# Kernel tuning notes

Hardware: AMD Instinct MI355X
Metric: run time of the kernel (lower is better)

## Reference

```python
import jax, jax.numpy as jnp
import numpy as np

N_NODES = 100000
N_EDGES = 1600000
F_IN = 128
HID = 128
N_CLASSES = 32
N_GRAPHS = 1024


def setup_inputs() -> dict:
    key = jax.random.key(0)
    ks = jax.random.split(key, 8)
    x = jax.random.normal(ks[0], (N_NODES, F_IN), dtype=jnp.float32)
    edge_index = jax.random.randint(ks[1], (2, N_EDGES), 0, N_NODES, dtype=jnp.int64)
    batch = jnp.sort(jax.random.randint(ks[2], (N_NODES,), 0, N_GRAPHS, dtype=jnp.int64))
    W1 = jax.random.normal(ks[3], (F_IN, HID), dtype=jnp.float32) * (1.0 / np.sqrt(F_IN))
    b1 = jnp.zeros((HID,), dtype=jnp.float32)
    W2 = jax.random.normal(ks[4], (HID, HID), dtype=jnp.float32) * (1.0 / np.sqrt(HID))
    b2 = jnp.zeros((HID,), dtype=jnp.float32)
    Wf = jax.random.normal(ks[5], (HID, N_CLASSES), dtype=jnp.float32) * (1.0 / np.sqrt(HID))
    bf = jnp.zeros((N_CLASSES,), dtype=jnp.float32)
    return {"x": x, "edge_index": edge_index, "batch": batch,
            "W1": W1, "b1": b1, "W2": W2, "b2": b2, "Wf": Wf, "bf": bf}


def _gcn_conv(x, W, b, src, dst, n_nodes):
    # GCNConv: linear transform, add self-loops, symmetric normalization,
    # scatter-add aggregation, then bias.
    h = x @ W                                   # [N, H]
    loop = jnp.arange(n_nodes, dtype=src.dtype)
    s = jnp.concatenate([src, loop])            # [E+N]
    d = jnp.concatenate([dst, loop])
    deg = jax.ops.segment_sum(jnp.ones_like(d, dtype=h.dtype), d, num_segments=n_nodes)
    dinv = jnp.where(deg > 0, jax.lax.rsqrt(deg), jnp.zeros_like(deg))
    norm = dinv[s] * dinv[d]                    # [E+N]
    msgs = h[s] * norm[:, None]                 # gather + scale
    out = jax.ops.segment_sum(msgs, d, num_segments=n_nodes)  # scatter-add
    return out + b


def reference(x, edge_index, batch, W1, b1, W2, b2, Wf, bf):
    src, dst = edge_index[0], edge_index[1]
    n = x.shape[0]
    h = _gcn_conv(x, W1, b1, src, dst, n)
    h = jax.nn.relu(h)
    # F.dropout(training=False) -> identity (inference baseline)
    h = _gcn_conv(h, W2, b2, src, dst, n)
    # global_mean_pool over graph ids
    pooled_sum = jax.ops.segment_sum(h, batch, num_segments=N_GRAPHS)       # [G, H]
    counts = jax.ops.segment_sum(jnp.ones((n,), h.dtype), batch, num_segments=N_GRAPHS)
    pooled = pooled_sum / jnp.clip(counts, 1.0)[:, None]
    return pooled @ Wf + bf                      # [G, C]
```

## Files before the change

### kernel.cpp

```cpp
#include <hip/hip_runtime.h>
#include <hip/hip_bf16.h>

#define N_NODES   100000
#define N_EDGES   1600000
#define FDIM      128
#define N_GRAPHS  1024
#define N_CLASSES 32
#define SCAN_BLK  1024
#define M_PAD     100032

typedef __attribute__((ext_vector_type(8))) short short8v;
typedef __attribute__((ext_vector_type(4))) float f32x4;

__device__ __forceinline__ float bflo(unsigned u){ union{unsigned i; float f;} c; c.i = u << 16; return c.f; }
__device__ __forceinline__ float bfhi(unsigned u){ union{unsigned i; float f;} c; c.i = u & 0xffff0000u; return c.f; }
__device__ __forceinline__ unsigned short f2bf(float f){
    union{float f; unsigned u;} c{f};
    return (unsigned short)((c.u + 0x7fffu + ((c.u >> 16) & 1u)) >> 16);
}
__device__ __forceinline__ unsigned packbf2(float a, float b){
    return (unsigned)f2bf(a) | ((unsigned)f2bf(b) << 16);
}

__device__ __forceinline__ void fma8(float* acc, float w, uint4 u) {
    acc[0] += w * bflo(u.x); acc[1] += w * bfhi(u.x);
    acc[2] += w * bflo(u.y); acc[3] += w * bfhi(u.y);
    acc[4] += w * bflo(u.z); acc[5] += w * bfhi(u.z);
    acc[6] += w * bflo(u.w); acc[7] += w * bfhi(u.w);
}

__global__ void k_f2bf(const float* __restrict__ in, unsigned* __restrict__ out, int n2) {
    int i = blockIdx.x * blockDim.x + threadIdx.x;
    if (i < n2) {
        float2 v = ((const float2*)in)[i];
        out[i] = packbf2(v.x, v.y);
    }
}

__global__ void k_wt(const float* __restrict__ W, unsigned short* __restrict__ Wt) {
    int i = blockIdx.x * blockDim.x + threadIdx.x;
    int k = i >> 7, n = i & 127;
    Wt[n * 128 + k] = f2bf(W[i]);
}

__global__ void k_count(const int* __restrict__ dst, int* __restrict__ indeg, int E) {
    int i = blockIdx.x * blockDim.x + threadIdx.x;
    if (i < E) atomicAdd(&indeg[dst[i]], 1);
}

__global__ void k_dinv(const int* __restrict__ indeg, float* __restrict__ dinv, int n) {
    int i = blockIdx.x * blockDim.x + threadIdx.x;
    if (i < n) dinv[i] = rsqrtf((float)(indeg[i] + 1));
}

__global__ void k_scan1(const int* __restrict__ in, int* __restrict__ out,
                        int* __restrict__ bsums, int n) {
    __shared__ int lds[256];
    int blk = blockIdx.x, t = threadIdx.x;
    int base = blk * SCAN_BLK + t * 4;
    int v[4];
#pragma unroll
    for (int i = 0; i < 4; ++i) v[i] = (base + i < n) ? in[base + i] : 0;
    int local = v[0] + v[1] + v[2] + v[3];
    lds[t] = local;
    __syncthreads();
    for (int off = 1; off < 256; off <<= 1) {
        int x = lds[t];
        int y = (t >= off) ? lds[t - off] : 0;
        __syncthreads();
        lds[t] = x + y;
        __syncthreads();
    }
    int excl = lds[t] - local;
    if (t == 255) bsums[blk] = lds[255];
    int run = excl;
#pragma unroll
    for (int i = 0; i < 4; ++i) {
        if (base + i < n) { out[base + i] = run; run += v[i]; }
    }
}

__global__ void k_scan2(int* __restrict__ bsums, int nb) {
    __shared__ int lds[256];
    int t = threadIdx.x;
    int orig = (t < nb) ? bsums[t] : 0;
    lds[t] = orig;
    __syncthreads();
    for (int off = 1; off < 256; off <<= 1) {
        int x = lds[t];
        int y = (t >= off) ? lds[t - off] : 0;
        __syncthreads();
        lds[t] = x + y;
        __syncthreads();
    }
    if (t < nb) bsums[t] = lds[t] - orig;
}

__global__ void k_scan3(int* __restrict__ rp, const int* __restrict__ boffs, int n, int E) {
    int i = blockIdx.x * blockDim.x + threadIdx.x;
    if (i < n) rp[i] += boffs[i / SCAN_BLK];
    if (i == n) rp[n] = E;
}

__global__ void k_fill(const int* __restrict__ src, const int* __restrict__ dst,
                       const int* __restrict__ rp, int* __restrict__ cursor,
                       int* __restrict__ col, float* __restrict__ wgt,
                       const float* __restrict__ dinv, int E) {
    int i = blockIdx.x * blockDim.x + threadIdx.x;
    if (i < E) {
        int d = dst[i], s = src[i];
        int p = atomicAdd(&cursor[d], 1);
        int idx = rp[d] + p;
        col[idx] = s;
        wgt[idx] = dinv[d] * dinv[s];
    }
}

#define AGG3_BODY(X2)                                                            \
    int lane = threadIdx.x & 63;                                                 \
    int grp  = lane >> 4;                                                        \
    int fl   = lane & 15;                                                        \
    int v = (blockIdx.x << 2) + (threadIdx.x >> 6);                              \
    if (v >= N_NODES) return;                                                    \
    float dv = dinv[v];                                                          \
    int e0 = rp[v];                                                              \
    int L  = rp[v + 1] - e0 + 1;                               \
    float acc[8] = {0.f,0.f,0.f,0.f,0.f,0.f,0.f,0.f};                            \
    int i = grp;                                                                 \
    int sA = -1, sB = -1; float wA = 0.f, wB = 0.f;                              \
    if (i < L) {                                                                 \
        if (i == 0) { sA = v; wA = dv * dv; }                                    \
        else        { sA = col[e0 + i - 1]; wA = wgt[e0 + i - 1]; }              \
    }                                                                            \
    if (i + 4 < L) { sB = col[e0 + i + 3]; wB = wgt[e0 + i + 3]; }               \
    while (sA >= 0) {                                                            \
        int sC = -1, sD = -1; float wC = 0.f, wD = 0.f;                          \
        if (i + 8  < L) { sC = col[e0 + i + 7];  wC = wgt[e0 + i + 7]; }         \
        if (i + 12 < L) { sD = col[e0 + i + 11]; wD = wgt[e0 + i + 11]; }        \
        uint4 uA = *(const uint4*)(X2 + (size_t)sA * 64 + fl * 4);               \
        uint4 uB;                                                                \
        bool hB = (sB >= 0);                                                     \
        if (hB) uB = *(const uint4*)(X2 + (size_t)sB * 64 + fl * 4);             \
        fma8(acc, wA, uA);                                                       \
        if (hB) fma8(acc, wB, uB);                                               \
        i += 8; sA = sC; wA = wC; sB = sD; wB = wD;                              \
    }                                                                            \
    _Pragma("unroll")                                                            \
    for (int j = 0; j < 8; ++j) {                                                \
        acc[j] += __shfl_xor(acc[j], 16, 64);                                    \
        acc[j] += __shfl_xor(acc[j], 32, 64);                                    \
    }

__global__ __launch_bounds__(256) void k_agg1(
    const unsigned* __restrict__ X2, unsigned* __restrict__ O2,
    const int* __restrict__ rp, const int* __restrict__ col,
    const float* __restrict__ wgt, const float* __restrict__ dinv)
{
    AGG3_BODY(X2)
    if (grp == 0) {
        uint4 o;
        o.x = packbf2(acc[0], acc[1]);
        o.y = packbf2(acc[2], acc[3]);
        o.z = packbf2(acc[4], acc[5]);
        o.w = packbf2(acc[6], acc[7]);
        *(uint4*)(O2 + (size_t)v * 64 + fl * 4) = o;
    }
}

__global__ __launch_bounds__(256) void k_agg2(
    const unsigned* __restrict__ X2,
    const int* __restrict__ rp, const int* __restrict__ col,
    const float* __restrict__ wgt, const float* __restrict__ dinv,
    const int* __restrict__ batch, float* __restrict__ P, int* __restrict__ cnt)
{
    AGG3_BODY(X2)
    int g = batch[v];
    atomicAdd(&P[(size_t)g * FDIM + fl * 8 + 2 * grp],     acc[2 * grp]);
    atomicAdd(&P[(size_t)g * FDIM + fl * 8 + 2 * grp + 1], acc[2 * grp + 1]);
    if (lane == 0) atomicAdd(&cnt[g], 1);
}

__global__ __launch_bounds__(256) void k_gemm_mfma(
    const unsigned short* __restrict__ A, const unsigned short* __restrict__ Wt,
    const float* __restrict__ bias, unsigned short* __restrict__ B)
{
    int lane = threadIdx.x & 63;
    int wv = threadIdx.x >> 6;
    size_t row0 = (size_t)blockIdx.x * 64 + (size_t)wv * 16;
    int r = lane & 15, g = lane >> 4;

    short8v af[4];
    const unsigned short* arow = A + (row0 + r) * FDIM + g * 8;
#pragma unroll
    for (int ks = 0; ks < 4; ++ks)
        af[ks] = *(const short8v*)(arow + ks * 32);

    f32x4 acc[8];
#pragma unroll
    for (int ct = 0; ct < 8; ++ct) {
        f32x4 a = {0.f, 0.f, 0.f, 0.f};
        const unsigned short* wrow = Wt + (ct * 16 + r) * FDIM + g * 8;
#pragma unroll
        for (int ks = 0; ks < 4; ++ks) {
            short8v bfr = *(const short8v*)(wrow + ks * 32);
            a = __builtin_amdgcn_mfma_f32_16x16x32_bf16(af[ks], bfr, a, 0, 0, 0);
        }
        acc[ct] = a;
    }

#pragma unroll
    for (int ct = 0; ct < 8; ++ct) {
        int c = ct * 16 + r;
        float bs = bias[c];
#pragma unroll
        for (int i = 0; i < 4; ++i) {
            size_t row = row0 + g * 4 + i;
            if (row < N_NODES) {
                float vv = fmaxf(acc[ct][i] + bs, 0.f);
                B[row * FDIM + c] = f2bf(vv);
            }
        }
    }
}

__global__ void k_wcomb(const float* __restrict__ W2, const float* __restrict__ Wf,
                        const float* __restrict__ b2, const float* __restrict__ bf,
                        float* __restrict__ Wc, float* __restrict__ bc) {
    int idx = blockIdx.x * blockDim.x + threadIdx.x;
    if (idx < 128 * 32) {
        int k = idx >> 5, c = idx & 31;
        float acc = 0.0f;
        for (int m = 0; m < 128; ++m) acc += W2[k * 128 + m] * Wf[m * 32 + c];
        Wc[idx] = acc;
    }
    if (idx < 32) {
        float acc = bf[idx];
        for (int m = 0; m < 128; ++m) acc += b2[m] * Wf[m * 32 + idx];
        bc[idx] = acc;
    }
}

__global__ void k_final(const float* __restrict__ P, const int* __restrict__ cnt,
                        const float* __restrict__ Wc, const float* __restrict__ bc,
                        const float* __restrict__ bf, float* __restrict__ out) {
    __shared__ float p[128];
    int g = blockIdx.x, t = threadIdx.x;
    int c_ = cnt[g];
    float inv = (c_ > 0) ? 1.0f / (float)c_ : 0.0f;
    p[t] = P[(size_t)g * FDIM + t] * inv;
    __syncthreads();
    if (t < N_CLASSES) {
        float acc = (c_ > 0) ? bc[t] : bf[t];
#pragma unroll
        for (int k = 0; k < 128; ++k) acc = fmaf(p[k], Wc[k * 32 + t], acc);
        out[(size_t)g * N_CLASSES + t] = acc;
    }
}

extern "C" void kernel_launch(void* const* d_in, const int* in_sizes, int n_in,
                              void* d_out, int out_size, void* d_ws, size_t ws_size,
                              hipStream_t stream) {
    const float* x    = (const float*)d_in[0];
    const int*   ei   = (const int*)d_in[1];
    const int*   batch= (const int*)d_in[2];
    const float* W1   = (const float*)d_in[3];
    const float* b1   = (const float*)d_in[4];
    const float* W2   = (const float*)d_in[5];
    const float* b2   = (const float*)d_in[6];
    const float* Wf   = (const float*)d_in[7];
    const float* bf   = (const float*)d_in[8];
    const int* src = ei;
    const int* dst = ei + N_EDGES;

    char* w = (char*)d_ws;
    auto alloc = [&](size_t bytes) { char* p = w; w += (bytes + 255) & ~255ull; return p; };
    int*      indeg  = (int*)     alloc((size_t)N_NODES * 4);
    float*    dinv   = (float*)   alloc((size_t)N_NODES * 4);
    int*      rp     = (int*)     alloc((size_t)(N_NODES + 1) * 4);
    int*      cursor = (int*)     alloc((size_t)N_NODES * 4);
    int*      bsums  = (int*)     alloc(1024 * 4);
    int*      col    = (int*)     alloc((size_t)N_EDGES * 4);
    float*    wgt    = (float*)   alloc((size_t)N_EDGES * 4);
    unsigned* xh     = (unsigned*)alloc((size_t)N_NODES * 64 * 4);
    unsigned* Ab     = (unsigned*)alloc((size_t)M_PAD  * 64 * 4);
    unsigned* Bb     = (unsigned*)alloc((size_t)N_NODES * 64 * 4);
    unsigned short* Wt = (unsigned short*)alloc(128 * 128 * 2);
    float*    P      = (float*)   alloc((size_t)N_GRAPHS * FDIM * 4);
    int*      cnt    = (int*)     alloc((size_t)N_GRAPHS * 4);
    float*    Wc     = (float*)   alloc(128 * 32 * 4);
    float*    bc     = (float*)   alloc(32 * 4);

    hipMemsetAsync(indeg,  0, (size_t)N_NODES * 4, stream);
    hipMemsetAsync(cursor, 0, (size_t)N_NODES * 4, stream);
    hipMemsetAsync(P,      0, (size_t)N_GRAPHS * FDIM * 4, stream);
    hipMemsetAsync(cnt,    0, (size_t)N_GRAPHS * 4, stream);

    const int nbScan = (N_NODES + SCAN_BLK - 1) / SCAN_BLK;

    k_f2bf<<<(N_NODES * 64 + 255) / 256, 256, 0, stream>>>(x, xh, N_NODES * 64);
    k_wt  <<<64, 256, 0, stream>>>(W1, Wt);

    k_count<<<(N_EDGES + 255) / 256, 256, 0, stream>>>(dst, indeg, N_EDGES);
    k_dinv <<<(N_NODES + 255) / 256, 256, 0, stream>>>(indeg, dinv, N_NODES);
    k_scan1<<<nbScan, 256, 0, stream>>>(indeg, rp, bsums, N_NODES);
    k_scan2<<<1, 256, 0, stream>>>(bsums, nbScan);
    k_scan3<<<(N_NODES + 1 + 255) / 256, 256, 0, stream>>>(rp, bsums, N_NODES, N_EDGES);
    k_fill <<<(N_EDGES + 255) / 256, 256, 0, stream>>>(src, dst, rp, cursor, col, wgt, dinv, N_EDGES);

    k_agg1<<<(N_NODES + 3) / 4, 256, 0, stream>>>(xh, Ab, rp, col, wgt, dinv);
    k_gemm_mfma<<<M_PAD / 64, 256, 0, stream>>>((const unsigned short*)Ab, Wt, b1,
                                                (unsigned short*)Bb);

    k_wcomb<<<16, 256, 0, stream>>>(W2, Wf, b2, bf, Wc, bc);

    k_agg2<<<(N_NODES + 3) / 4, 256, 0, stream>>>(Bb, rp, col, wgt, dinv, batch, P, cnt);

    k_final<<<N_GRAPHS, 128, 0, stream>>>(P, cnt, Wc, bc, bf, (float*)d_out);
}
```

Measured before the change: 492.5 us.

## Slice feature matrices into 8 column slabs and interleave CSR edge records

Node feature arrays are stored as eight 16-feature slices, each contiguous across nodes. The aggregation kernels become one block per (4-node group, slice), so each pass over a slice gathers from a 3.2 MB working set that may stay in cache. Column indices and edge weights are packed into one 8-byte record read with nontemporal loads, and the GEMM reads and writes the sliced layout. The trade-off is that edge lists are traversed eight times, each gather is only 32 bytes per row, and there are many more blocks.

```diff
diff --git a/kernel.cpp b/kernel.cpp
--- a/kernel.cpp
+++ b/kernel.cpp
@@ -8,6 +8,7 @@
 #define N_CLASSES 32
 #define SCAN_BLK  1024
 #define M_PAD     100032
+#define SLICE_U   (M_PAD * 8)
 
 typedef __attribute__((ext_vector_type(8))) short short8v;
 typedef __attribute__((ext_vector_type(4))) float f32x4;
@@ -21,19 +22,17 @@
 __device__ __forceinline__ unsigned packbf2(float a, float b){
     return (unsigned)f2bf(a) | ((unsigned)f2bf(b) << 16);
 }
-
-__device__ __forceinline__ void fma8(float* acc, float w, uint4 u) {
-    acc[0] += w * bflo(u.x); acc[1] += w * bfhi(u.x);
-    acc[2] += w * bflo(u.y); acc[3] += w * bfhi(u.y);
-    acc[4] += w * bflo(u.z); acc[5] += w * bfhi(u.z);
-    acc[6] += w * bflo(u.w); acc[7] += w * bfhi(u.w);
+__device__ __forceinline__ long long ldnt64(const void* p){
+    return __builtin_nontemporal_load((const long long*)p);
 }
 
 __global__ void k_f2bf(const float* __restrict__ in, unsigned* __restrict__ out, int n2) {
     int i = blockIdx.x * blockDim.x + threadIdx.x;
     if (i < n2) {
-        float2 v = ((const float2*)in)[i];
-        out[i] = packbf2(v.x, v.y);
+        float2 v2 = ((const float2*)in)[i];
+        int v = i >> 6, jp = i & 63;
+        int f = jp >> 3, off = jp & 7;
+        out[(size_t)f * SLICE_U + (size_t)v * 8 + off] = packbf2(v2.x, v2.y);
     }
 }
 
@@ -104,80 +103,75 @@
 
 __global__ void k_fill(const int* __restrict__ src, const int* __restrict__ dst,
                        const int* __restrict__ rp, int* __restrict__ cursor,
-                       int* __restrict__ col, float* __restrict__ wgt,
-                       const float* __restrict__ dinv, int E) {
+                       int2* __restrict__ edges, const float* __restrict__ dinv, int E) {
     int i = blockIdx.x * blockDim.x + threadIdx.x;
     if (i < E) {
         int d = dst[i], s = src[i];
         int p = atomicAdd(&cursor[d], 1);
-        int idx = rp[d] + p;
-        col[idx] = s;
-        wgt[idx] = dinv[d] * dinv[s];
-    }
-}
-
-#define AGG3_BODY(X2)                                                            \
+        int2 r; r.x = s; r.y = __float_as_int(dinv[d] * dinv[s]);
+        edges[rp[d] + p] = r;
+    }
+}
+
+#define AGGS_BODY(X2)                                                            \
     int lane = threadIdx.x & 63;                                                 \
-    int grp  = lane >> 4;                                                        \
-    int fl   = lane & 15;                                                        \
-    int v = (blockIdx.x << 2) + (threadIdx.x >> 6);                              \
-    if (v >= N_NODES) return;                                                    \
+    int wv   = threadIdx.x >> 6;                                                 \
+    int f    = blockIdx.x & 7;                                                   \
+    int v    = ((blockIdx.x >> 3) << 2) + wv;                                    \
+    int grp  = lane >> 3;                                                        \
+    int fl   = lane & 7;                                                         \
+    const unsigned* Xs = X2 + (size_t)f * SLICE_U;                               \
     float dv = dinv[v];                                                          \
-    int e0 = rp[v];                                                              \
-    int L  = rp[v + 1] - e0 + 1;                               \
-    float acc[8] = {0.f,0.f,0.f,0.f,0.f,0.f,0.f,0.f};                            \
+    int e0 = rp[v], deg = rp[v + 1] - e0;                                        \
+    float a0 = 0.f, a1 = 0.f;                                                    \
+    if (grp == 0) {                                                              \
+        unsigned u = Xs[(size_t)v * 8 + fl];                                     \
+        float ws = dv * dv;                                                      \
+        a0 = ws * bflo(u); a1 = ws * bfhi(u);                                    \
+    }                                                                            \
     int i = grp;                                                                 \
-    int sA = -1, sB = -1; float wA = 0.f, wB = 0.f;                              \
-    if (i < L) {                                                                 \
-        if (i == 0) { sA = v; wA = dv * dv; }                                    \
-        else        { sA = col[e0 + i - 1]; wA = wgt[e0 + i - 1]; }              \
-    }                                                                            \
-    if (i + 4 < L) { sB = col[e0 + i + 3]; wB = wgt[e0 + i + 3]; }               \
-    while (sA >= 0) {                                                            \
-        int sC = -1, sD = -1; float wC = 0.f, wD = 0.f;                          \
-        if (i + 8  < L) { sC = col[e0 + i + 7];  wC = wgt[e0 + i + 7]; }         \
-        if (i + 12 < L) { sD = col[e0 + i + 11]; wD = wgt[e0 + i + 11]; }        \
-        uint4 uA = *(const uint4*)(X2 + (size_t)sA * 64 + fl * 4);               \
-        uint4 uB;                                                                \
-        bool hB = (sB >= 0);                                                     \
-        if (hB) uB = *(const uint4*)(X2 + (size_t)sB * 64 + fl * 4);             \
-        fma8(acc, wA, uA);                                                       \
-        if (hB) fma8(acc, wB, uB);                                               \
-        i += 8; sA = sC; wA = wC; sB = sD; wB = wD;                              \
+    bool h0 = (i < deg);                                                         \
+    long long rec = 0;                                                           \
+    if (h0) rec = ldnt64(edges + e0 + i);                                        \
+    while (h0) {                                                                 \
+        bool h1 = (i + 8 < deg);                                                 \
+        long long rec1 = 0;                                                      \
+        if (h1) rec1 = ldnt64(edges + e0 + i + 8);                               \
+        int s   = (int)(rec & 0xffffffffll);                                     \
+        float w = __int_as_float((int)(rec >> 32));                              \
+        unsigned u = Xs[(size_t)s * 8 + fl];                                     \
+        a0 += w * bflo(u); a1 += w * bfhi(u);                                    \
+        i += 8; rec = rec1; h0 = h1;                                             \
     }                                                                            \
     _Pragma("unroll")                                                            \
-    for (int j = 0; j < 8; ++j) {                                                \
-        acc[j] += __shfl_xor(acc[j], 16, 64);                                    \
-        acc[j] += __shfl_xor(acc[j], 32, 64);                                    \
-    }
-
-__global__ __launch_bounds__(256) void k_agg1(
+    for (int off = 8; off < 64; off <<= 1) {                                     \
+        a0 += __shfl_xor(a0, off, 64);                                           \
+        a1 += __shfl_xor(a1, off, 64);                                           \
+    }
+
+__global__ __launch_bounds__(256) void k_aggs1(
     const unsigned* __restrict__ X2, unsigned* __restrict__ O2,
-    const int* __restrict__ rp, const int* __restrict__ col,
-    const float* __restrict__ wgt, const float* __restrict__ dinv)
+    const int* __restrict__ rp, const int2* __restrict__ edges,
+    const float* __restrict__ dinv)
 {
-    AGG3_BODY(X2)
+    AGGS_BODY(X2)
+    if (grp == 0)
+        O2[(size_t)f * SLICE_U + (size_t)v * 8 + fl] = packbf2(a0, a1);
+}
+
+__global__ __launch_bounds__(256) void k_aggs2(
+    const unsigned* __restrict__ X2,
+    const int* __restrict__ rp, const int2* __restrict__ edges,
+    const float* __restrict__ dinv, const int* __restrict__ batch,
+    float* __restrict__ P, int* __restrict__ cnt)
+{
+    AGGS_BODY(X2)
+    int g = batch[v];
     if (grp == 0) {
-        uint4 o;
-        o.x = packbf2(acc[0], acc[1]);
-        o.y = packbf2(acc[2], acc[3]);
-        o.z = packbf2(acc[4], acc[5]);
-        o.w = packbf2(acc[6], acc[7]);
-        *(uint4*)(O2 + (size_t)v * 64 + fl * 4) = o;
-    }
-}
-
-__global__ __launch_bounds__(256) void k_agg2(
-    const unsigned* __restrict__ X2,
-    const int* __restrict__ rp, const int* __restrict__ col,
-    const float* __restrict__ wgt, const float* __restrict__ dinv,
-    const int* __restrict__ batch, float* __restrict__ P, int* __restrict__ cnt)
-{
-    AGG3_BODY(X2)
-    int g = batch[v];
-    atomicAdd(&P[(size_t)g * FDIM + fl * 8 + 2 * grp],     acc[2 * grp]);
-    atomicAdd(&P[(size_t)g * FDIM + fl * 8 + 2 * grp + 1], acc[2 * grp + 1]);
-    if (lane == 0) atomicAdd(&cnt[g], 1);
+        atomicAdd(&P[(size_t)g * FDIM + f * 16 + fl * 2],     a0);
+        atomicAdd(&P[(size_t)g * FDIM + f * 16 + fl * 2 + 1], a1);
+    }
+    if (f == 0 && lane == 0) atomicAdd(&cnt[g], 1);
 }
 
 __global__ __launch_bounds__(256) void k_gemm_mfma(
@@ -190,10 +184,12 @@
     int r = lane & 15, g = lane >> 4;
 
     short8v af[4];
-    const unsigned short* arow = A + (row0 + r) * FDIM + g * 8;
-#pragma unroll
-    for (int ks = 0; ks < 4; ++ks)
-        af[ks] = *(const short8v*)(arow + ks * 32);
+#pragma unroll
+    for (int ks = 0; ks < 4; ++ks) {
+        int fa  = 2 * ks + (g >> 1);
+        int off = (g & 1) * 8;
+        af[ks] = *(const short8v*)(A + (size_t)fa * SLICE_U * 2 + (row0 + r) * 16 + off);
+    }
 
     f32x4 acc[8];
 #pragma unroll
@@ -210,14 +206,13 @@
 
 #pragma unroll
     for (int ct = 0; ct < 8; ++ct) {
-        int c = ct * 16 + r;
-        float bs = bias[c];
+        float bs = bias[ct * 16 + r];
 #pragma unroll
         for (int i = 0; i < 4; ++i) {
             size_t row = row0 + g * 4 + i;
             if (row < N_NODES) {
                 float vv = fmaxf(acc[ct][i] + bs, 0.f);
-                B[row * FDIM + c] = f2bf(vv);
+                B[(size_t)ct * SLICE_U * 2 + row * 16 + r] = f2bf(vv);
             }
         }
     }
@@ -279,11 +274,10 @@
     int*      rp     = (int*)     alloc((size_t)(N_NODES + 1) * 4);
     int*      cursor = (int*)     alloc((size_t)N_NODES * 4);
     int*      bsums  = (int*)     alloc(1024 * 4);
-    int*      col    = (int*)     alloc((size_t)N_EDGES * 4);
-    float*    wgt    = (float*)   alloc((size_t)N_EDGES * 4);
-    unsigned* xh     = (unsigned*)alloc((size_t)N_NODES * 64 * 4);
-    unsigned* Ab     = (unsigned*)alloc((size_t)M_PAD  * 64 * 4);
-    unsigned* Bb     = (unsigned*)alloc((size_t)N_NODES * 64 * 4);
+    int2*     edges  = (int2*)    alloc((size_t)N_EDGES * 8);
+    unsigned* xh     = (unsigned*)alloc((size_t)SLICE_U * 8 * 4);
+    unsigned* Ab     = (unsigned*)alloc((size_t)SLICE_U * 8 * 4);
+    unsigned* Bb     = (unsigned*)alloc((size_t)SLICE_U * 8 * 4);
     unsigned short* Wt = (unsigned short*)alloc(128 * 128 * 2);
     float*    P      = (float*)   alloc((size_t)N_GRAPHS * FDIM * 4);
     int*      cnt    = (int*)     alloc((size_t)N_GRAPHS * 4);
@@ -305,15 +299,15 @@
     k_scan1<<<nbScan, 256, 0, stream>>>(indeg, rp, bsums, N_NODES);
     k_scan2<<<1, 256, 0, stream>>>(bsums, nbScan);
     k_scan3<<<(N_NODES + 1 + 255) / 256, 256, 0, stream>>>(rp, bsums, N_NODES, N_EDGES);
-    k_fill <<<(N_EDGES + 255) / 256, 256, 0, stream>>>(src, dst, rp, cursor, col, wgt, dinv, N_EDGES);
-
-    k_agg1<<<(N_NODES + 3) / 4, 256, 0, stream>>>(xh, Ab, rp, col, wgt, dinv);
+    k_fill <<<(N_EDGES + 255) / 256, 256, 0, stream>>>(src, dst, rp, cursor, edges, dinv, N_EDGES);
+
+    k_aggs1<<<(N_NODES / 4) * 8, 256, 0, stream>>>(xh, Ab, rp, edges, dinv);
     k_gemm_mfma<<<M_PAD / 64, 256, 0, stream>>>((const unsigned short*)Ab, Wt, b1,
                                                 (unsigned short*)Bb);
 
     k_wcomb<<<16, 256, 0, stream>>>(W2, Wf, b2, bf, Wc, bc);
 
-    k_agg2<<<(N_NODES + 3) / 4, 256, 0, stream>>>(Bb, rp, col, wgt, dinv, batch, P, cnt);
+    k_aggs2<<<(N_NODES / 4) * 8, 256, 0, stream>>>(Bb, rp, edges, dinv, batch, P, cnt);
 
     k_final<<<N_GRAPHS, 128, 0, stream>>>(P, cnt, Wc, bc, bf, (float*)d_out);
 }
```

New measurement: 1.536 ms. +211.8%, slower.

## Replace second-layer aggregation with source-ordered scatter-to-graph pooling

Applied to the files above, without the earlier changes.

The second GCN layer is only needed through its mean pool, so the pooled sum is computed directly as a weighted sum of source-node features into graph bins. A source-sorted edge list (including self-loops) holds packed weight and destination-graph id, and chunked blocks accumulate into LDS before a partial-sum reduction. This removes the per-node gather-aggregate pass and its global atomics. In exchange it adds an out-degree count, a second scan and fill pass, larger workspace, and packs the graph id into the low mantissa bits of the weight, which slightly perturbs precision.

```diff
diff --git a/kernel.cpp b/kernel.cpp
--- a/kernel.cpp
+++ b/kernel.cpp
@@ -8,6 +8,8 @@
 #define N_CLASSES 32
 #define SCAN_BLK  1024
 #define M_PAD     100032
+#define CHUNK     1563
+#define NCHUNK    64
 
 typedef __attribute__((ext_vector_type(8))) short short8v;
 typedef __attribute__((ext_vector_type(4))) float f32x4;
@@ -21,6 +23,9 @@
 __device__ __forceinline__ unsigned packbf2(float a, float b){
     return (unsigned)f2bf(a) | ((unsigned)f2bf(b) << 16);
 }
+__device__ __forceinline__ int packgw(float w, int g){
+    return (__float_as_int(w) & ~1023) | g;
+}
 
 __device__ __forceinline__ void fma8(float* acc, float w, uint4 u) {
     acc[0] += w * bflo(u.x); acc[1] += w * bfhi(u.x);
@@ -43,14 +48,19 @@
     Wt[n * 128 + k] = f2bf(W[i]);
 }
 
-__global__ void k_count(const int* __restrict__ dst, int* __restrict__ indeg, int E) {
-    int i = blockIdx.x * blockDim.x + threadIdx.x;
-    if (i < E) atomicAdd(&indeg[dst[i]], 1);
+__global__ void k_count(const int* __restrict__ idx, int* __restrict__ deg, int E) {
+    int i = blockIdx.x * blockDim.x + threadIdx.x;
+    if (i < E) atomicAdd(&deg[idx[i]], 1);
 }
 
 __global__ void k_dinv(const int* __restrict__ indeg, float* __restrict__ dinv, int n) {
     int i = blockIdx.x * blockDim.x + threadIdx.x;
     if (i < n) dinv[i] = rsqrtf((float)(indeg[i] + 1));
+}
+
+__global__ void k_p1(int* __restrict__ a, int n) {
+    int i = blockIdx.x * blockDim.x + threadIdx.x;
+    if (i < n) a[i] += 1;
 }
 
 __global__ void k_scan1(const int* __restrict__ in, int* __restrict__ out,
@@ -96,10 +106,10 @@
     if (t < nb) bsums[t] = lds[t] - orig;
 }
 
-__global__ void k_scan3(int* __restrict__ rp, const int* __restrict__ boffs, int n, int E) {
+__global__ void k_scan3(int* __restrict__ rp, const int* __restrict__ boffs, int n, int TOT) {
     int i = blockIdx.x * blockDim.x + threadIdx.x;
     if (i < n) rp[i] += boffs[i / SCAN_BLK];
-    if (i == n) rp[n] = E;
+    if (i == n) rp[n] = TOT;
 }
 
 __global__ void k_fill(const int* __restrict__ src, const int* __restrict__ dst,
@@ -116,47 +126,72 @@
     }
 }
 
-#define AGG3_BODY(X2)                                                            \
-    int lane = threadIdx.x & 63;                                                 \
-    int grp  = lane >> 4;                                                        \
-    int fl   = lane & 15;                                                        \
-    int v = (blockIdx.x << 2) + (threadIdx.x >> 6);                              \
-    if (v >= N_NODES) return;                                                    \
-    float dv = dinv[v];                                                          \
-    int e0 = rp[v];                                                              \
-    int L  = rp[v + 1] - e0 + 1;                               \
-    float acc[8] = {0.f,0.f,0.f,0.f,0.f,0.f,0.f,0.f};                            \
-    int i = grp;                                                                 \
-    int sA = -1, sB = -1; float wA = 0.f, wB = 0.f;                              \
-    if (i < L) {                                                                 \
-        if (i == 0) { sA = v; wA = dv * dv; }                                    \
-        else        { sA = col[e0 + i - 1]; wA = wgt[e0 + i - 1]; }              \
-    }                                                                            \
-    if (i + 4 < L) { sB = col[e0 + i + 3]; wB = wgt[e0 + i + 3]; }               \
-    while (sA >= 0) {                                                            \
-        int sC = -1, sD = -1; float wC = 0.f, wD = 0.f;                          \
-        if (i + 8  < L) { sC = col[e0 + i + 7];  wC = wgt[e0 + i + 7]; }         \
-        if (i + 12 < L) { sD = col[e0 + i + 11]; wD = wgt[e0 + i + 11]; }        \
-        uint4 uA = *(const uint4*)(X2 + (size_t)sA * 64 + fl * 4);               \
-        uint4 uB;                                                                \
-        bool hB = (sB >= 0);                                                     \
-        if (hB) uB = *(const uint4*)(X2 + (size_t)sB * 64 + fl * 4);             \
-        fma8(acc, wA, uA);                                                       \
-        if (hB) fma8(acc, wB, uB);                                               \
-        i += 8; sA = sC; wA = wC; sB = sD; wB = wD;                              \
-    }                                                                            \
-    _Pragma("unroll")                                                            \
-    for (int j = 0; j < 8; ++j) {                                                \
-        acc[j] += __shfl_xor(acc[j], 16, 64);                                    \
-        acc[j] += __shfl_xor(acc[j], 32, 64);                                    \
-    }
+__global__ void k_selfrec(const int* __restrict__ rps, const int* __restrict__ batch,
+                          const float* __restrict__ dinv, int2* __restrict__ recs, int n) {
+    int v = blockIdx.x * blockDim.x + threadIdx.x;
+    if (v < n) {
+        float dv = dinv[v];
+        int2 r; r.x = v; r.y = packgw(dv * dv, batch[v]);
+        recs[rps[v]] = r;
+    }
+}
+
+__global__ void k_fill2(const int* __restrict__ src, const int* __restrict__ dst,
+                        const int* __restrict__ rps, int* __restrict__ cursor2,
+                        const int* __restrict__ batch, const float* __restrict__ dinv,
+                        int2* __restrict__ recs, int E) {
+    int i = blockIdx.x * blockDim.x + threadIdx.x;
+    if (i < E) {
+        int s = src[i], d = dst[i];
+        int p = atomicAdd(&cursor2[s], 1);
+        int2 r; r.x = s; r.y = packgw(dinv[s] * dinv[d], batch[d]);
+        recs[rps[s] + 1 + p] = r;
+    }
+}
+
+__global__ void k_cnt(const int* __restrict__ batch, int* __restrict__ cnt, int n) {
+    int i = blockIdx.x * blockDim.x + threadIdx.x;
+    if (i < n) atomicAdd(&cnt[batch[i]], 1);
+}
 
 __global__ __launch_bounds__(256) void k_agg1(
     const unsigned* __restrict__ X2, unsigned* __restrict__ O2,
     const int* __restrict__ rp, const int* __restrict__ col,
     const float* __restrict__ wgt, const float* __restrict__ dinv)
 {
-    AGG3_BODY(X2)
+    int lane = threadIdx.x & 63;
+    int grp  = lane >> 4;
+    int fl   = lane & 15;
+    int v = (blockIdx.x << 2) + (threadIdx.x >> 6);
+    if (v >= N_NODES) return;
+    float dv = dinv[v];
+    int e0 = rp[v];
+    int L  = rp[v + 1] - e0 + 1;
+    float acc[8] = {0.f,0.f,0.f,0.f,0.f,0.f,0.f,0.f};
+    int i = grp;
+    int sA = -1, sB = -1; float wA = 0.f, wB = 0.f;
+    if (i < L) {
+        if (i == 0) { sA = v; wA = dv * dv; }
+        else        { sA = col[e0 + i - 1]; wA = wgt[e0 + i - 1]; }
+    }
+    if (i + 4 < L) { sB = col[e0 + i + 3]; wB = wgt[e0 + i + 3]; }
+    while (sA >= 0) {
+        int sC = -1, sD = -1; float wC = 0.f, wD = 0.f;
+        if (i + 8  < L) { sC = col[e0 + i + 7];  wC = wgt[e0 + i + 7]; }
+        if (i + 12 < L) { sD = col[e0 + i + 11]; wD = wgt[e0 + i + 11]; }
+        uint4 uA = *(const uint4*)(X2 + (size_t)sA * 64 + fl * 4);
+        uint4 uB;
+        bool hB = (sB >= 0);
+        if (hB) uB = *(const uint4*)(X2 + (size_t)sB * 64 + fl * 4);
+        fma8(acc, wA, uA);
+        if (hB) fma8(acc, wB, uB);
+        i += 8; sA = sC; wA = wC; sB = sD; wB = wD;
+    }
+#pragma unroll
+    for (int j = 0; j < 8; ++j) {
+        acc[j] += __shfl_xor(acc[j], 16, 64);
+        acc[j] += __shfl_xor(acc[j], 32, 64);
+    }
     if (grp == 0) {
         uint4 o;
         o.x = packbf2(acc[0], acc[1]);
@@ -165,19 +200,6 @@
         o.w = packbf2(acc[6], acc[7]);
         *(uint4*)(O2 + (size_t)v * 64 + fl * 4) = o;
     }
-}
-
-__global__ __launch_bounds__(256) void k_agg2(
-    const unsigned* __restrict__ X2,
-    const int* __restrict__ rp, const int* __restrict__ col,
-    const float* __restrict__ wgt, const float* __restrict__ dinv,
-    const int* __restrict__ batch, float* __restrict__ P, int* __restrict__ cnt)
-{
-    AGG3_BODY(X2)
-    int g = batch[v];
-    atomicAdd(&P[(size_t)g * FDIM + fl * 8 + 2 * grp],     acc[2 * grp]);
-    atomicAdd(&P[(size_t)g * FDIM + fl * 8 + 2 * grp + 1], acc[2 * grp + 1]);
-    if (lane == 0) atomicAdd(&cnt[g], 1);
 }
 
 __global__ __launch_bounds__(256) void k_gemm_mfma(
@@ -221,6 +243,60 @@
             }
         }
     }
+}
+
+__global__ __launch_bounds__(512) void k_pool(
+    const unsigned* __restrict__ H2, const int2* __restrict__ recs,
+    const int* __restrict__ rps, float* __restrict__ Ppart)
+{
+    __shared__ float pl[N_GRAPHS][32];
+    int c = blockIdx.x >> 2;
+    int q = blockIdx.x & 3;
+    int t = threadIdx.x;
+    for (int i = t; i < N_GRAPHS * 32; i += 512) ((float*)pl)[i] = 0.f;
+    __syncthreads();
+
+    int v0 = c * CHUNK, v1 = min(v0 + CHUNK, N_NODES);
+    int e0 = rps[v0], e1 = rps[v1];
+    int f  = t & 31;
+    int uo = q * 16 + (f >> 1);
+    bool hi = (f & 1);
+
+    int e = e0 + (t >> 5);
+    if (e < e1) {
+        int2 r = recs[e];
+        unsigned u = H2[(size_t)r.x * 64 + uo];
+        for (;;) {
+            int en = e + 16;
+            bool more = (en < e1);
+            int2 rn; unsigned un;
+            if (more) {
+                rn = recs[en];
+                un = H2[(size_t)rn.x * 64 + uo];
+            }
+            int g = r.y & 1023;
+            float w = __int_as_float(r.y & ~1023);
+            atomicAdd(&pl[g][f], w * (hi ? bfhi(u) : bflo(u)));
+            if (!more) break;
+            e = en; r = rn; u = un;
+        }
+    }
+    __syncthreads();
+    float* dst = Ppart + ((size_t)(q * NCHUNK + c)) * (N_GRAPHS * 32);
+    for (int i = t; i < N_GRAPHS * 32; i += 512) dst[i] = ((float*)pl)[i];
+}
+
+__global__ void k_pred(const float* __restrict__ Ppart, float* __restrict__ P) {
+    int i = blockIdx.x * blockDim.x + threadIdx.x;
+    if (i >= N_GRAPHS * FDIM) return;
+    int f = i & 127, g = i >> 7;
+    int q = f >> 5, j = f & 31;
+    float acc = 0.f;
+    const float* base = Ppart + ((size_t)q * NCHUNK) * (N_GRAPHS * 32) + (size_t)g * 32 + j;
+#pragma unroll 4
+    for (int c = 0; c < NCHUNK; ++c)
+        acc += base[(size_t)c * (N_GRAPHS * 32)];
+    P[i] = acc;
 }
 
 __global__ void k_wcomb(const float* __restrict__ W2, const float* __restrict__ Wf,
@@ -275,25 +351,31 @@
     char* w = (char*)d_ws;
     auto alloc = [&](size_t bytes) { char* p = w; w += (bytes + 255) & ~255ull; return p; };
     int*      indeg  = (int*)     alloc((size_t)N_NODES * 4);
+    int*      odeg   = (int*)     alloc((size_t)N_NODES * 4);
     float*    dinv   = (float*)   alloc((size_t)N_NODES * 4);
     int*      rp     = (int*)     alloc((size_t)(N_NODES + 1) * 4);
+    int*      rps    = (int*)     alloc((size_t)(N_NODES + 1) * 4);
     int*      cursor = (int*)     alloc((size_t)N_NODES * 4);
+    int*      cursor2= (int*)     alloc((size_t)N_NODES * 4);
     int*      bsums  = (int*)     alloc(1024 * 4);
     int*      col    = (int*)     alloc((size_t)N_EDGES * 4);
     float*    wgt    = (float*)   alloc((size_t)N_EDGES * 4);
+    int2*     recs   = (int2*)    alloc((size_t)(N_EDGES + N_NODES) * 8);
     unsigned* xh     = (unsigned*)alloc((size_t)N_NODES * 64 * 4);
     unsigned* Ab     = (unsigned*)alloc((size_t)M_PAD  * 64 * 4);
     unsigned* Bb     = (unsigned*)alloc((size_t)N_NODES * 64 * 4);
     unsigned short* Wt = (unsigned short*)alloc(128 * 128 * 2);
+    float*    Ppart  = (float*)   alloc((size_t)4 * NCHUNK * N_GRAPHS * 32 * 4);
     float*    P      = (float*)   alloc((size_t)N_GRAPHS * FDIM * 4);
     int*      cnt    = (int*)     alloc((size_t)N_GRAPHS * 4);
     float*    Wc     = (float*)   alloc(128 * 32 * 4);
     float*    bc     = (float*)   alloc(32 * 4);
 
-    hipMemsetAsync(indeg,  0, (size_t)N_NODES * 4, stream);
-    hipMemsetAsync(cursor, 0, (size_t)N_NODES * 4, stream);
-    hipMemsetAsync(P,      0, (size_t)N_GRAPHS * FDIM * 4, stream);
-    hipMemsetAsync(cnt,    0, (size_t)N_GRAPHS * 4, stream);
+    hipMemsetAsync(indeg,   0, (size_t)N_NODES * 4, stream);
+    hipMemsetAsync(odeg,    0, (size_t)N_NODES * 4, stream);
+    hipMemsetAsync(cursor,  0, (size_t)N_NODES * 4, stream);
+    hipMemsetAsync(cursor2, 0, (size_t)N_NODES * 4, stream);
+    hipMemsetAsync(cnt,     0, (size_t)N_GRAPHS * 4, stream);
 
     const int nbScan = (N_NODES + SCAN_BLK - 1) / SCAN_BLK;
 
@@ -301,11 +383,21 @@
     k_wt  <<<64, 256, 0, stream>>>(W1, Wt);
 
     k_count<<<(N_EDGES + 255) / 256, 256, 0, stream>>>(dst, indeg, N_EDGES);
+    k_count<<<(N_EDGES + 255) / 256, 256, 0, stream>>>(src, odeg, N_EDGES);
     k_dinv <<<(N_NODES + 255) / 256, 256, 0, stream>>>(indeg, dinv, N_NODES);
+    k_p1   <<<(N_NODES + 255) / 256, 256, 0, stream>>>(odeg, N_NODES);
+
     k_scan1<<<nbScan, 256, 0, stream>>>(indeg, rp, bsums, N_NODES);
     k_scan2<<<1, 256, 0, stream>>>(bsums, nbScan);
     k_scan3<<<(N_NODES + 1 + 255) / 256, 256, 0, stream>>>(rp, bsums, N_NODES, N_EDGES);
-    k_fill <<<(N_EDGES + 255) / 256, 256, 0, stream>>>(src, dst, rp, cursor, col, wgt, dinv, N_EDGES);
+    k_scan1<<<nbScan, 256, 0, stream>>>(odeg, rps, bsums, N_NODES);
+    k_scan2<<<1, 256, 0, stream>>>(bsums, nbScan);
+    k_scan3<<<(N_NODES + 1 + 255) / 256, 256, 0, stream>>>(rps, bsums, N_NODES, N_EDGES + N_NODES);
+
+    k_fill   <<<(N_EDGES + 255) / 256, 256, 0, stream>>>(src, dst, rp, cursor, col, wgt, dinv, N_EDGES);
+    k_selfrec<<<(N_NODES + 255) / 256, 256, 0, stream>>>(rps, batch, dinv, recs, N_NODES);
+    k_fill2  <<<(N_EDGES + 255) / 256, 256, 0, stream>>>(src, dst, rps, cursor2, batch, dinv, recs, N_EDGES);
+    k_cnt    <<<(N_NODES + 255) / 256, 256, 0, stream>>>(batch, cnt, N_NODES);
 
     k_agg1<<<(N_NODES + 3) / 4, 256, 0, stream>>>(xh, Ab, rp, col, wgt, dinv);
     k_gemm_mfma<<<M_PAD / 64, 256, 0, stream>>>((const unsigned short*)Ab, Wt, b1,
@@ -313,7 +405,8 @@
 
     k_wcomb<<<16, 256, 0, stream>>>(W2, Wf, b2, bf, Wc, bc);
 
-    k_agg2<<<(N_NODES + 3) / 4, 256, 0, stream>>>(Bb, rp, col, wgt, dinv, batch, P, cnt);
+    k_pool<<<NCHUNK * 4, 512, 0, stream>>>(Bb, recs, rps, Ppart);
+    k_pred<<<(N_GRAPHS * FDIM + 255) / 256, 256, 0, stream>>>(Ppart, P);
 
     k_final<<<N_GRAPHS, 128, 0, stream>>>(P, cnt, Wc, bc, bf, (float*)d_out);
 }
```

Result: slower. 1.722 ms (+249.6%).
